# Kernel optimization log

Measured on AMD Instinct MI355X. Metric: run time of the kernel, lower is better.

The kernel has to match this reference:

```python
import jax, jax.numpy as jnp
import numpy as np

DIM = 256
HEADS = 8
DIM_HEAD = 32
HIDDEN = HEADS * DIM_HEAD  # 256
SCALE = DIM_HEAD ** -0.5


def setup_inputs() -> dict:
    key = jax.random.key(0)
    k1, k2, k3, k4 = jax.random.split(key, 4)
    x = jax.random.normal(k1, (1, DIM, 16, 16, 16), dtype=jnp.float32)
    # 1x1x1 Conv3d weights are plain channel-mixing matrices
    w_qkv = jax.random.normal(k2, (3 * HIDDEN, DIM), dtype=jnp.float32) * (DIM ** -0.5)
    w_out = jax.random.normal(k3, (DIM, HIDDEN), dtype=jnp.float32) * (HIDDEN ** -0.5)
    b_out = jax.random.normal(k4, (DIM,), dtype=jnp.float32) * 0.01
    return {"x": x, "w_qkv": w_qkv, "w_out": w_out, "b_out": b_out}


def reference(x, w_qkv, w_out, b_out):
    b, c, X, Y, Z = x.shape
    n = X * Y * Z
    xf = x.reshape(b, c, n)                                   # b c n
    qkv = jnp.einsum('oc,bcn->bon', w_qkv, xf)                # b 3H n
    q, k, v = jnp.split(qkv, 3, axis=1)                       # each b (h c) n
    def heads(t):
        return t.reshape(b, HEADS, DIM_HEAD, n)               # b h c n
    q, k, v = heads(q) * SCALE, heads(k), heads(v)
    sim = jnp.einsum('bhci,bhcj->bhij', q, k)                 # b h n n
    attn = jax.nn.softmax(sim, axis=-1)
    out = jnp.einsum('bhij,bhcj->bhci', attn, v)              # b h c n
    out = out.reshape(b, HIDDEN, n)                           # b (h c) n
    out = jnp.einsum('oc,bcn->bon', w_out, out) + b_out[None, :, None]
    return out.reshape(b, DIM, X, Y, Z)
```

## Files before the change

kernel.cpp:

```cpp
#include <hip/hip_runtime.h>
#include <hip/hip_bf16.h>
#include <cstdint>


typedef __bf16 bf16x8 __attribute__((ext_vector_type(8)));
typedef float f32x4 __attribute__((ext_vector_type(4)));
typedef float f32x16 __attribute__((ext_vector_type(16)));
typedef unsigned int u32;
typedef unsigned short u16;
typedef u32 u32x4v __attribute__((ext_vector_type(4)));
typedef u32 u32x2v __attribute__((ext_vector_type(2)));

#define MFMA16(a, b, c) __builtin_amdgcn_mfma_f32_16x16x32_bf16(a, b, c, 0, 0, 0)
#define MFMA32(a, b, c) __builtin_amdgcn_mfma_f32_32x32x16_bf16(a, b, c, 0, 0, 0)

#if __has_builtin(__builtin_amdgcn_exp2f)
#define EXP2(x) __builtin_amdgcn_exp2f(x)
#else
#define EXP2(x) exp2f(x)
#endif

__device__ __forceinline__ u16 f2bf(float f) {
  __bf16 b = (__bf16)f;
  return __builtin_bit_cast(u16, b);
}
__device__ __forceinline__ u32 pk2(float a, float b) {
  return (u32)f2bf(a) | ((u32)f2bf(b) << 16);
}
__device__ __forceinline__ bf16x8 ldfrag(const u16* p) {
  return __builtin_bit_cast(bf16x8, *(const u32x4v*)p);
}
__device__ __forceinline__ void gload_lds16(const void* g, void* l) {
  __builtin_amdgcn_global_load_lds((const __attribute__((address_space(1))) u32*)g,
                                   (__attribute__((address_space(3))) u32*)l, 16, 0, 0);
}
__device__ __forceinline__ void plswap(u32& a, u32& b) {
  asm("v_permlane32_swap_b32 %0, %1" : "+v"(a), "+v"(b));
}
__device__ __forceinline__ f32x16 zero16() {
  f32x16 z;
#pragma unroll
  for (int i = 0; i < 16; ++i) z[i] = 0.0f;
  return z;
}

#if __has_builtin(__builtin_amdgcn_fdot2_f32_bf16)
typedef __bf16 bf16x2 __attribute__((ext_vector_type(2)));
__device__ __forceinline__ float dot2one(u32 pk, float acc) {
  const u32 one2 = 0x3F803F80u;
  return __builtin_amdgcn_fdot2_f32_bf16(__builtin_bit_cast(bf16x2, pk),
                                         __builtin_bit_cast(bf16x2, one2), acc, false);
}
#define LSUM4(LSUM, PK0, PK1, PK2, PK3) \
  LSUM = dot2one(PK0, LSUM);            \
  LSUM = dot2one(PK1, LSUM);            \
  LSUM = dot2one(PK2, LSUM);            \
  LSUM = dot2one(PK3, LSUM);
#define LSUM_F32(LSUM, ...)
#else
#define LSUM4(LSUM, PK0, PK1, PK2, PK3)
#define LSUM_F32(LSUM, P0, P1, P2, P3, P4, P5, P6, P7) \
  LSUM += ((P0 + P1) + (P2 + P3)) + ((P4 + P5) + (P6 + P7));
#endif

__global__ __launch_bounds__(256) void prep(const float* __restrict__ x,
                                            const float* __restrict__ wq,
                                            const float* __restrict__ wo,
                                            u16* __restrict__ xT, u16* __restrict__ wqb,
                                            u16* __restrict__ wob) {
  const int b = blockIdx.x;
  const int t = threadIdx.x;
  if (b < 256) {
    __shared__ u16 tile[64][72];
    const int n0 = (b & 63) * 64, c0 = (b >> 6) * 64;
#pragma unroll
    for (int r = 0; r < 4; ++r) {
      int c = r * 16 + (t >> 4);
      int n4 = (t & 15) << 2;
      float4 v = *(const float4*)(x + (size_t)(c0 + c) * 4096 + n0 + n4);
      tile[n4 + 0][c] = f2bf(v.x);
      tile[n4 + 1][c] = f2bf(v.y);
      tile[n4 + 2][c] = f2bf(v.z);
      tile[n4 + 3][c] = f2bf(v.w);
    }
    __syncthreads();
#pragma unroll
    for (int r2 = 0; r2 < 2; ++r2) {
      int n = r2 * 32 + (t >> 3);
      int c8 = (t & 7) << 3;
      u32x4v o;
#pragma unroll
      for (int j = 0; j < 4; ++j)
        o[j] = (u32)tile[n][c8 + 2 * j] | ((u32)tile[n][c8 + 2 * j + 1] << 16);
      *(u32x4v*)(xT + (size_t)(n0 + n) * 256 + c0 + c8) = o;
    }
  } else if (b < 304) {
    int base = (b - 256) * 4096;
#pragma unroll
    for (int r = 0; r < 4; ++r) {
      int i = base + r * 1024 + t * 4;
      float4 v = *(const float4*)(wq + i);
      float sc = (i < 65536) ? 0.2550349f : 1.0f;
      u32x2v pkd;
      pkd.x = pk2(v.x * sc, v.y * sc);
      pkd.y = pk2(v.z * sc, v.w * sc);
      *(u32x2v*)(wqb + i) = pkd;
    }
  } else {
    int base = (b - 304) * 4096;
#pragma unroll
    for (int r = 0; r < 4; ++r) {
      int i = base + r * 1024 + t * 4;
      float4 v = *(const float4*)(wo + i);
      u32x2v pkd;
      pkd.x = pk2(v.x, v.y);
      pkd.y = pk2(v.z, v.w);
      *(u32x2v*)(wob + i) = pkd;
    }
  }
}

__global__ __launch_bounds__(256) void qkv_gemm(const u16* __restrict__ xT,
                                                const u16* __restrict__ wqb,
                                                u16* __restrict__ qT, u16* __restrict__ kT,
                                                u16* __restrict__ vv) {
  __shared__ __align__(16) u16 Al[64 * 64];
  __shared__ __align__(16) u16 Bl[64 * 64];
  const int t = threadIdx.x;
  const int lane = t & 63, w = t >> 6;
  const int wm = w & 1, wn = w >> 1;
  const int o0 = blockIdx.y * 64, n0 = blockIdx.x * 64;
  const int lr = lane & 15, lg = lane >> 4;
  const int srow = lane >> 3, sslot = lane & 7;
  f32x4 acc[2][2];
#pragma unroll
  for (int i = 0; i < 2; ++i)
#pragma unroll
    for (int j = 0; j < 2; ++j)
#pragma unroll
      for (int r = 0; r < 4; ++r) acc[i][j][r] = 0.0f;

  for (int kc = 0; kc < 256; kc += 64) {
#pragma unroll
    for (int rnd = 0; rnd < 2; ++rnd) {
      int row = rnd * 32 + w * 8 + srow;
      gload_lds16(wqb + (size_t)(o0 + row) * 256 + kc + ((sslot ^ (row & 7)) << 3),
                  (void*)(Al + rnd * 2048 + w * 512));
      gload_lds16(xT + (size_t)(n0 + row) * 256 + kc + ((sslot ^ (row & 7)) << 3),
                  (void*)(Bl + rnd * 2048 + w * 512));
    }
    __syncthreads();
#pragma unroll
    for (int kk = 0; kk < 2; ++kk) {
      bf16x8 af[2], bf_[2];
#pragma unroll
      for (int mi = 0; mi < 2; ++mi) {
        int row = wm * 32 + mi * 16 + lr;
        af[mi] = ldfrag(&Al[row * 64 + ((kk * 32 + lg * 8) ^ ((row & 7) << 3))]);
      }
#pragma unroll
      for (int ni = 0; ni < 2; ++ni) {
        int row = wn * 32 + ni * 16 + lr;
        bf_[ni] = ldfrag(&Bl[row * 64 + ((kk * 32 + lg * 8) ^ ((row & 7) << 3))]);
      }
#pragma unroll
      for (int mi = 0; mi < 2; ++mi)
#pragma unroll
        for (int ni = 0; ni < 2; ++ni) acc[mi][ni] = MFMA16(af[mi], bf_[ni], acc[mi][ni]);
    }
    __syncthreads();
  }
#pragma unroll
  for (int mi = 0; mi < 2; ++mi) {
#pragma unroll
    for (int ni = 0; ni < 2; ++ni) {
      int obase = o0 + wm * 32 + mi * 16 + lg * 4;
      int n = n0 + wn * 32 + ni * 16 + lr;
      int part = obase >> 8;
      int oin = obase & 255;
      int h = oin >> 5, c0 = oin & 31;
      if (part == 0) {
        u32x2v pv;
        pv.x = pk2(acc[mi][ni][0], acc[mi][ni][1]);
        pv.y = pk2(acc[mi][ni][2], acc[mi][ni][3]);
        *(u32x2v*)(qT + ((size_t)h * 4096 + n) * 32 + c0) = pv;
      } else if (part == 1) {
        u32x2v pv;
        pv.x = pk2(acc[mi][ni][0], acc[mi][ni][1]);
        pv.y = pk2(acc[mi][ni][2], acc[mi][ni][3]);
        *(u32x2v*)(kT + ((size_t)h * 4096 + n) * 32 + c0) = pv;
      } else {
#pragma unroll
        for (int r = 0; r < 4; ++r)
          vv[((size_t)h * 32 + c0 + r) * 4096 + n] = f2bf(acc[mi][ni][r]);
      }
    }
  }
}


#define QK2(ST, QA, QB, K0, K1)         \
  do {                                  \
    ST = zero16();                      \
    __builtin_amdgcn_s_setprio(1);      \
    ST = MFMA32(K0, QA, ST);            \
    ST = MFMA32(K1, QB, ST);            \
    __builtin_amdgcn_s_setprio(0);      \
  } while (0)

#define SM_PV(ST, LO, OACC, LSUM, VF)                                           \
  do {                                                                          \
    float p0_ = EXP2(ST[LO + 0]), p1_ = EXP2(ST[LO + 1]);                       \
    float p2_ = EXP2(ST[LO + 2]), p3_ = EXP2(ST[LO + 3]);                       \
    float p4_ = EXP2(ST[LO + 4]), p5_ = EXP2(ST[LO + 5]);                       \
    float p6_ = EXP2(ST[LO + 6]), p7_ = EXP2(ST[LO + 7]);                       \
    u32 k0_ = pk2(p0_, p1_), k1_ = pk2(p2_, p3_);                               \
    u32 k2_ = pk2(p4_, p5_), k3_ = pk2(p6_, p7_);                               \
    LSUM4(LSUM, k0_, k1_, k2_, k3_)                                             \
    LSUM_F32(LSUM, p0_, p1_, p2_, p3_, p4_, p5_, p6_, p7_)                      \
    u32 ax_ = k0_, bx_ = k2_;                                                   \
    plswap(ax_, bx_);                                                           \
    u32 ay_ = k1_, by_ = k3_;                                                   \
    plswap(ay_, by_);                                                           \
    u32x4v f_;                                                                  \
    f_.x = ax_; f_.y = ay_; f_.z = bx_; f_.w = by_;                             \
    __builtin_amdgcn_s_setprio(1);                                              \
    OACC = MFMA32(VF, __builtin_bit_cast(bf16x8, f_), OACC);                    \
    __builtin_amdgcn_s_setprio(0);                                              \
  } while (0)

#define STAGE(TT, VF0, VF1)                                   \
  do {                                                        \
    SM_PV(sTa, 0, oacc0, lsum0, VF0);                         \
    SM_PV(sTa, 8, oacc0, lsum0, VF1);                         \
    QK2(sTa, qf00, qf01, kfn0, kfn1);                         \
    SM_PV(sTb, 0, oacc1, lsum1, VF0);                         \
    SM_PV(sTb, 8, oacc1, lsum1, VF1);                         \
    QK2(sTb, qf10, qf11, kfn0, kfn1);                         \
    kfn0 = ldfrag(kp0 + (TT + 2) * 1024);                     \
    kfn1 = ldfrag(kp0 + (TT + 2) * 1024 + 16);                \
    VF0 = ldfrag(vp0 + (TT + 2) * 32);                        \
    VF1 = ldfrag(vp0 + (TT + 2) * 32 + 16);                   \
  } while (0)

__global__ __launch_bounds__(512, 4) void attn_fused(const u16* __restrict__ qT,
                                                     const u16* __restrict__ kT,
                                                     const u16* __restrict__ vv,
                                                     u16* __restrict__ aout) {
  __shared__ float pbuf[8 * 32 * 66];
  __shared__ float lbuf[8 * 64];
  const int tid = threadIdx.x;
  const int lane = tid & 63, s = tid >> 6;
  const int h = blockIdx.x & 7, qb = blockIdx.x >> 3;
  const int l31 = lane & 31, lh = lane >> 5;
  const u16* qTh = qT + (size_t)h * (4096 * 32);
  const u16* kTh = kT + (size_t)h * (4096 * 32);
  const u16* vh = vv + (size_t)h * (32 * 4096);

  const int i0 = qb * 64 + l31;
  bf16x8 qf00 = ldfrag(qTh + (size_t)i0 * 32 + lh * 8);
  bf16x8 qf01 = ldfrag(qTh + (size_t)i0 * 32 + 16 + lh * 8);
  bf16x8 qf10 = ldfrag(qTh + (size_t)(i0 + 32) * 32 + lh * 8);
  bf16x8 qf11 = ldfrag(qTh + (size_t)(i0 + 32) * 32 + 16 + lh * 8);

  f32x16 oacc0 = zero16(), oacc1 = zero16();
  float lsum0 = 0.0f, lsum1 = 0.0f;
  const int kvbase = s * 512;

  const u16* kp0 = kTh + (size_t)(kvbase + l31) * 32 + lh * 8;
  const u16* vp0 = vh + (size_t)l31 * 4096 + kvbase + lh * 8;

  bf16x8 kc0 = ldfrag(kp0), kc1 = ldfrag(kp0 + 16);
  bf16x8 vfa0 = ldfrag(vp0), vfa1 = ldfrag(vp0 + 16);
  bf16x8 kfn0 = ldfrag(kp0 + 1024), kfn1 = ldfrag(kp0 + 1024 + 16);
  bf16x8 vfb0 = ldfrag(vp0 + 32), vfb1 = ldfrag(vp0 + 32 + 16);
  f32x16 sTa, sTb;
  QK2(sTa, qf00, qf01, kc0, kc1);
  QK2(sTb, qf10, qf11, kc0, kc1);

#pragma unroll
  for (int tt = 0; tt < 16; tt += 2) {
    STAGE(tt, vfa0, vfa1);
    STAGE(tt + 1, vfb0, vfb1);
  }

  float ls0 = lsum0 + __shfl_xor(lsum0, 32, 64);
  float ls1 = lsum1 + __shfl_xor(lsum1, 32, 64);
#pragma unroll
  for (int r = 0; r < 16; ++r) {
    int c = (r & 3) + 8 * (r >> 2) + 4 * lh;
    pbuf[(s * 32 + c) * 66 + l31] = oacc0[r];
    pbuf[(s * 32 + c) * 66 + 32 + l31] = oacc1[r];
  }
  lbuf[s * 64 + l31] = ls0;
  lbuf[s * 64 + 32 + l31] = ls1;
  __syncthreads();

  {
    int i = tid >> 3, c0 = (tid & 7) << 2;
    float lt = 0.0f;
#pragma unroll
    for (int ss = 0; ss < 8; ++ss) lt += lbuf[ss * 64 + i];
    float inv = 1.0f / lt;
    float a[4];
#pragma unroll
    for (int cc = 0; cc < 4; ++cc) a[cc] = 0.0f;
#pragma unroll
    for (int ss = 0; ss < 8; ++ss)
#pragma unroll
      for (int cc = 0; cc < 4; ++cc) a[cc] += pbuf[(ss * 32 + c0 + cc) * 66 + i];
    u32x2v ov;
    ov.x = pk2(a[0] * inv, a[1] * inv);
    ov.y = pk2(a[2] * inv, a[3] * inv);
    *(u32x2v*)(aout + (size_t)(qb * 64 + i) * 256 + h * 32 + c0) = ov;
  }
}

__global__ __launch_bounds__(256) void out_proj(const u16* __restrict__ wob,
                                                const float* __restrict__ bo,
                                                const u16* __restrict__ aout,
                                                float* __restrict__ out) {
  __shared__ __align__(16) u16 Al[64 * 64];
  __shared__ __align__(16) u16 Bl[64 * 64];
  const int t = threadIdx.x;
  const int lane = t & 63, w = t >> 6;
  const int n0 = blockIdx.x * 64, d0 = blockIdx.y * 64;
  const int lr = lane & 15, lg = lane >> 4;
  const int srow = lane >> 3, sslot = lane & 7;
  f32x4 acc[4];
#pragma unroll
  for (int ni = 0; ni < 4; ++ni)
#pragma unroll
    for (int r = 0; r < 4; ++r) acc[ni][r] = 0.0f;

  for (int kc = 0; kc < 256; kc += 64) {
#pragma unroll
    for (int rnd = 0; rnd < 2; ++rnd) {
      int row = rnd * 32 + w * 8 + srow;
      gload_lds16(wob + (size_t)(d0 + row) * 256 + kc + ((sslot ^ (row & 7)) << 3),
                  (void*)(Al + rnd * 2048 + w * 512));
      gload_lds16(aout + (size_t)(n0 + row) * 256 + kc + ((sslot ^ (row & 7)) << 3),
                  (void*)(Bl + rnd * 2048 + w * 512));
    }
    __syncthreads();
#pragma unroll
    for (int kk = 0; kk < 2; ++kk) {
      int arow = w * 16 + lr;
      bf16x8 af = ldfrag(&Al[arow * 64 + ((kk * 32 + lg * 8) ^ ((arow & 7) << 3))]);
#pragma unroll
      for (int ni = 0; ni < 4; ++ni) {
        int brow = ni * 16 + lr;
        bf16x8 bfr = ldfrag(&Bl[brow * 64 + ((kk * 32 + lg * 8) ^ ((brow & 7) << 3))]);
        acc[ni] = MFMA16(af, bfr, acc[ni]);
      }
    }
    __syncthreads();
  }
#pragma unroll
  for (int ni = 0; ni < 4; ++ni) {
    int n = n0 + ni * 16 + lr;
#pragma unroll
    for (int r = 0; r < 4; ++r) {
      int d = d0 + w * 16 + lg * 4 + r;
      out[(size_t)d * 4096 + n] = acc[ni][r] + bo[d];
    }
  }
}

extern "C" void kernel_launch(void* const* d_in, const int* in_sizes, int n_in,
                              void* d_out, int out_size, void* d_ws, size_t ws_size,
                              hipStream_t stream) {
  (void)in_sizes; (void)n_in; (void)out_size; (void)ws_size;
  const float* x = (const float*)d_in[0];
  const float* wqkv = (const float*)d_in[1];
  const float* wout = (const float*)d_in[2];
  const float* bout = (const float*)d_in[3];
  float* out = (float*)d_out;
  u16* qT = (u16*)d_ws;
  u16* kT = qT + 8 * 4096 * 32;
  u16* vv = kT + 8 * 4096 * 32;
  u16* aout = vv + 8 * 32 * 4096;
  u16* xT = aout + 4096 * 256;
  u16* wqb = xT + 4096 * 256;
  u16* wob = wqb + 768 * 256;

  prep<<<320, 256, 0, stream>>>(x, wqkv, wout, xT, wqb, wob);
  qkv_gemm<<<dim3(64, 12), 256, 0, stream>>>(xT, wqb, qT, kT, vv);
  attn_fused<<<512, 512, 0, stream>>>(qT, kT, vv, aout);
  out_proj<<<dim3(64, 4), 256, 0, stream>>>(wob, bout, aout, out);
}
```

Measured before the change: 48.35 us.

## Double-buffer LDS tiles in QKV and output projection GEMMs

Both projection GEMM kernels now hold two LDS buffers per operand. The global-to-LDS load for the next K chunk is issued before computing on the current one, with explicit vmcnt waits and raw s_barriers in place of __syncthreads. The goal is to overlap global memory latency with MFMA work in these small K=256 GEMMs. It doubles LDS use per block (32KB), which could lower occupancy, and it depends on the vmcnt count of 4 matching the number of outstanding loads.

```diff
diff --git a/kernel.cpp b/kernel.cpp
--- a/kernel.cpp
+++ b/kernel.cpp
@@ -124,8 +124,8 @@
                                                 const u16* __restrict__ wqb,
                                                 u16* __restrict__ qT, u16* __restrict__ kT,
                                                 u16* __restrict__ vv) {
-  __shared__ __align__(16) u16 Al[64 * 64];
-  __shared__ __align__(16) u16 Bl[64 * 64];
+  __shared__ __align__(16) u16 Al[2][64 * 64];
+  __shared__ __align__(16) u16 Bl[2][64 * 64];
   const int t = threadIdx.x;
   const int lane = t & 63, w = t >> 6;
   const int wm = w & 1, wn = w >> 1;
@@ -140,35 +140,53 @@
 #pragma unroll
       for (int r = 0; r < 4; ++r) acc[i][j][r] = 0.0f;
 
-  for (int kc = 0; kc < 256; kc += 64) {
-#pragma unroll
-    for (int rnd = 0; rnd < 2; ++rnd) {
-      int row = rnd * 32 + w * 8 + srow;
-      gload_lds16(wqb + (size_t)(o0 + row) * 256 + kc + ((sslot ^ (row & 7)) << 3),
-                  (void*)(Al + rnd * 2048 + w * 512));
-      gload_lds16(xT + (size_t)(n0 + row) * 256 + kc + ((sslot ^ (row & 7)) << 3),
-                  (void*)(Bl + rnd * 2048 + w * 512));
-    }
-    __syncthreads();
+#define QKV_STAGE(KI, BUF)                                                                   \
+  do {                                                                                       \
+    _Pragma("unroll") for (int rnd = 0; rnd < 2; ++rnd) {                                    \
+      int row = rnd * 32 + w * 8 + srow;                                                     \
+      gload_lds16(wqb + (size_t)(o0 + row) * 256 + (KI) * 64 + ((sslot ^ (row & 7)) << 3),   \
+                  (void*)(&Al[BUF][rnd * 2048 + w * 512]));                                  \
+      gload_lds16(xT + (size_t)(n0 + row) * 256 + (KI) * 64 + ((sslot ^ (row & 7)) << 3),    \
+                  (void*)(&Bl[BUF][rnd * 2048 + w * 512]));                                  \
+    }                                                                                        \
+  } while (0)
+
+  QKV_STAGE(0, 0);
+#pragma unroll
+  for (int ki = 0; ki < 4; ++ki) {
+    if (ki < 3) {
+      QKV_STAGE(ki + 1, (ki + 1) & 1);
+      asm volatile("s_waitcnt vmcnt(4)" ::: "memory");
+    } else {
+      asm volatile("s_waitcnt vmcnt(0)" ::: "memory");
+    }
+    __builtin_amdgcn_sched_barrier(0);
+    __builtin_amdgcn_s_barrier();
+    asm volatile("" ::: "memory");
+    const u16* Ab = &Al[ki & 1][0];
+    const u16* Bb = &Bl[ki & 1][0];
 #pragma unroll
     for (int kk = 0; kk < 2; ++kk) {
       bf16x8 af[2], bf_[2];
 #pragma unroll
       for (int mi = 0; mi < 2; ++mi) {
         int row = wm * 32 + mi * 16 + lr;
-        af[mi] = ldfrag(&Al[row * 64 + ((kk * 32 + lg * 8) ^ ((row & 7) << 3))]);
+        af[mi] = ldfrag(&Ab[row * 64 + ((kk * 32 + lg * 8) ^ ((row & 7) << 3))]);
       }
 #pragma unroll
       for (int ni = 0; ni < 2; ++ni) {
         int row = wn * 32 + ni * 16 + lr;
-        bf_[ni] = ldfrag(&Bl[row * 64 + ((kk * 32 + lg * 8) ^ ((row & 7) << 3))]);
+        bf_[ni] = ldfrag(&Bb[row * 64 + ((kk * 32 + lg * 8) ^ ((row & 7) << 3))]);
       }
 #pragma unroll
       for (int mi = 0; mi < 2; ++mi)
 #pragma unroll
         for (int ni = 0; ni < 2; ++ni) acc[mi][ni] = MFMA16(af[mi], bf_[ni], acc[mi][ni]);
     }
-    __syncthreads();
+    asm volatile("s_waitcnt lgkmcnt(0)" ::: "memory");
+    __builtin_amdgcn_sched_barrier(0);
+    __builtin_amdgcn_s_barrier();
+    asm volatile("" ::: "memory");
   }
 #pragma unroll
   for (int mi = 0; mi < 2; ++mi) {
@@ -320,8 +338,8 @@
                                                 const float* __restrict__ bo,
                                                 const u16* __restrict__ aout,
                                                 float* __restrict__ out) {
-  __shared__ __align__(16) u16 Al[64 * 64];
-  __shared__ __align__(16) u16 Bl[64 * 64];
+  __shared__ __align__(16) u16 Al[2][64 * 64];
+  __shared__ __align__(16) u16 Bl[2][64 * 64];
   const int t = threadIdx.x;
   const int lane = t & 63, w = t >> 6;
   const int n0 = blockIdx.x * 64, d0 = blockIdx.y * 64;
@@ -333,28 +351,46 @@
 #pragma unroll
     for (int r = 0; r < 4; ++r) acc[ni][r] = 0.0f;
 
-  for (int kc = 0; kc < 256; kc += 64) {
-#pragma unroll
-    for (int rnd = 0; rnd < 2; ++rnd) {
-      int row = rnd * 32 + w * 8 + srow;
-      gload_lds16(wob + (size_t)(d0 + row) * 256 + kc + ((sslot ^ (row & 7)) << 3),
-                  (void*)(Al + rnd * 2048 + w * 512));
-      gload_lds16(aout + (size_t)(n0 + row) * 256 + kc + ((sslot ^ (row & 7)) << 3),
-                  (void*)(Bl + rnd * 2048 + w * 512));
-    }
-    __syncthreads();
+#define PROJ_STAGE(KI, BUF)                                                                  \
+  do {                                                                                       \
+    _Pragma("unroll") for (int rnd = 0; rnd < 2; ++rnd) {                                    \
+      int row = rnd * 32 + w * 8 + srow;                                                     \
+      gload_lds16(wob + (size_t)(d0 + row) * 256 + (KI) * 64 + ((sslot ^ (row & 7)) << 3),   \
+                  (void*)(&Al[BUF][rnd * 2048 + w * 512]));                                  \
+      gload_lds16(aout + (size_t)(n0 + row) * 256 + (KI) * 64 + ((sslot ^ (row & 7)) << 3),  \
+                  (void*)(&Bl[BUF][rnd * 2048 + w * 512]));                                  \
+    }                                                                                        \
+  } while (0)
+
+  PROJ_STAGE(0, 0);
+#pragma unroll
+  for (int ki = 0; ki < 4; ++ki) {
+    if (ki < 3) {
+      PROJ_STAGE(ki + 1, (ki + 1) & 1);
+      asm volatile("s_waitcnt vmcnt(4)" ::: "memory");
+    } else {
+      asm volatile("s_waitcnt vmcnt(0)" ::: "memory");
+    }
+    __builtin_amdgcn_sched_barrier(0);
+    __builtin_amdgcn_s_barrier();
+    asm volatile("" ::: "memory");
+    const u16* Ab = &Al[ki & 1][0];
+    const u16* Bb = &Bl[ki & 1][0];
 #pragma unroll
     for (int kk = 0; kk < 2; ++kk) {
       int arow = w * 16 + lr;
-      bf16x8 af = ldfrag(&Al[arow * 64 + ((kk * 32 + lg * 8) ^ ((arow & 7) << 3))]);
+      bf16x8 af = ldfrag(&Ab[arow * 64 + ((kk * 32 + lg * 8) ^ ((arow & 7) << 3))]);
 #pragma unroll
       for (int ni = 0; ni < 4; ++ni) {
         int brow = ni * 16 + lr;
-        bf16x8 bfr = ldfrag(&Bl[brow * 64 + ((kk * 32 + lg * 8) ^ ((brow & 7) << 3))]);
+        bf16x8 bfr = ldfrag(&Bb[brow * 64 + ((kk * 32 + lg * 8) ^ ((brow & 7) << 3))]);
         acc[ni] = MFMA16(af, bfr, acc[ni]);
       }
     }
-    __syncthreads();
+    asm volatile("s_waitcnt lgkmcnt(0)" ::: "memory");
+    __builtin_amdgcn_sched_barrier(0);
+    __builtin_amdgcn_s_barrier();
+    asm volatile("" ::: "memory");
   }
 #pragma unroll
   for (int ni = 0; ni < 4; ++ni) {
```

After: 48.20 us, median of 2. No clear change (-0.3%).
